# Performance work log

Measured on AMD Instinct MI355X. Metric: run time of the kernel, lower is better.

The kernel has to match this reference:

```python
import jax, jax.numpy as jnp
import numpy as np

B, S, D, H = 4096, 200, 64, 36
BN_EPS = 1e-5
DICE_EPS = 1e-3


def setup_inputs() -> dict:
    key = jax.random.key(0)
    ks = jax.random.split(key, 6)
    return {
        "history": jax.random.normal(ks[0], (B, S, D), dtype=jnp.float32),
        "candidate": jax.random.normal(ks[1], (B, D), dtype=jnp.float32),
        "W1": jax.random.normal(ks[2], (4 * D, H), dtype=jnp.float32) * 0.05,
        "b1": jax.random.normal(ks[3], (H,), dtype=jnp.float32) * 0.05,
        "gamma": jnp.ones((H,), dtype=jnp.float32),
        "beta": jnp.zeros((H,), dtype=jnp.float32),
        "alpha": jax.random.normal(ks[4], (1,), dtype=jnp.float32),
        "W2": jax.random.normal(ks[5], (H, 1), dtype=jnp.float32) * 0.05,
        "b2": jnp.zeros((1,), dtype=jnp.float32),
    }


def reference(history, candidate, W1, b1, gamma, beta, alpha, W2, b2):
    b, s, d = history.shape
    cand = jnp.broadcast_to(candidate[:, None, :], (b, s, d))
    att_in = jnp.concatenate([cand, history, cand - history, cand * history], axis=-1)
    x = att_in.reshape(b * s, 4 * d)
    # Linear
    h = x @ W1 + b1
    # BatchNorm1d (training mode: batch statistics, biased variance)
    mu = h.mean(axis=0)
    var = h.var(axis=0)
    h = (h - mu) * jax.lax.rsqrt(var + BN_EPS) * gamma + beta
    # Dice: per-row normalization over features, eps=1e-3
    avg = h.mean(axis=1, keepdims=True)
    v = jnp.sum((h - avg) ** 2, axis=1, keepdims=True) / h.shape[1]
    ps = jax.nn.sigmoid((h - avg) / jnp.sqrt(v + DICE_EPS))
    h = ps * h + (1.0 - ps) * alpha * h
    # Output linear -> attention weight per (b, s)
    w = (h @ W2 + b2).reshape(b, s)
    # Weighted sum pooling over sequence
    return jnp.einsum("bs,bsd->bd", w, history)
```

## Files before the change

kernel.cpp:

```cpp
#include <hip/hip_runtime.h>
#include <hip/hip_bf16.h>
#include <math.h>

#define BB 4096
#define SS 200
#define DD 64
#define HH 36
#define NP 48
#define NROWSF (4096.0f * 200.0f)
#define NPB (2 * BB)
#define PSTRIDE 80

typedef short bf16x8 __attribute__((ext_vector_type(8)));
typedef float f32x4 __attribute__((ext_vector_type(4)));

__device__ __forceinline__ unsigned short f2bf(float f) {
    union { float f; unsigned u; } v; v.f = f;
    unsigned r = v.u + 0x7FFFu + ((v.u >> 16) & 1u);
    return (unsigned short)(r >> 16);
}
__device__ __forceinline__ unsigned f2bf2(float a, float b) {
    union { __hip_bfloat162 h; unsigned u; } v;
    v.h = __float22bfloat162_rn(float2{a, b});
    return v.u;
}

__device__ __forceinline__ void gl_lds16(const void* g, void* l) {
    __builtin_amdgcn_global_load_lds(
        (const __attribute__((address_space(1))) unsigned*)g,
        (__attribute__((address_space(3))) unsigned*)l, 16, 0, 0);
}

__global__ __launch_bounds__(256) void k_wb(const float* __restrict__ cand,
                                            const float* __restrict__ W1,
                                            const float* __restrict__ b1,
                                            unsigned short* __restrict__ WbG,
                                            float* __restrict__ baseG) {
    int b = blockIdx.x, t = threadIdx.x;
    __shared__ float shC[DD];
    if (t < DD) shC[t] = cand[b * DD + t];
    __syncthreads();
    unsigned short* wb = WbG + (size_t)b * (NP * DD);
#pragma unroll
    for (int u = 0; u < 12; ++u) {
        int e = t + u * 256;
        int n = e >> 6, k = e & 63;
        float val = 0.f;
        if (n < HH)
            val = W1[(DD + k) * HH + n] - W1[(2 * DD + k) * HH + n] +
                  shC[k] * W1[(3 * DD + k) * HH + n];
        wb[e] = f2bf(val);
    }
    if (t < NP) {
        float v = 0.f;
        if (t < HH) {
            v = b1[t];
            for (int k = 0; k < DD; ++k)
                v += shC[k] * (W1[k * HH + t] + W1[(2 * DD + k) * HH + t]);
        }
        baseG[b * NP + t] = v;
    }
}

template <bool WB>
__device__ __forceinline__ void prologue(int b, int half, int t,
                                         const float* __restrict__ hist,
                                         const float* __restrict__ cand,
                                         const float* __restrict__ W1,
                                         const float* __restrict__ b1,
                                         const unsigned short* __restrict__ WbG,
                                         const float* __restrict__ baseG,
                                         float* shHf, unsigned short* shWbT,
                                         float* shC, float* shBase,
                                         float (*shBaseP)[NP]) {
    int w = t >> 6, l = t & 63;
    const float* hsrc = hist + ((size_t)b * SS + (half ? 112 : 0)) * DD;
    if (WB) {
        const char* hb = (const char*)hsrc;
        char* lb = (char*)shHf;
#pragma unroll
        for (int u = 0; u < 7; ++u) {
            int j = w * 7 + u;
            if (!half || j < 22)
                gl_lds16(hb + j * 1024 + l * 16, lb + j * 1024 + l * 16);
        }
        const char* wbsrc = (const char*)(WbG + (size_t)b * (NP * DD));
        char* wbl = (char*)shWbT;
        gl_lds16(wbsrc + w * 1024 + l * 16, wbl + w * 1024 + l * 16);
        if (w < 2)
            gl_lds16(wbsrc + (4 + w) * 1024 + l * 16, wbl + (4 + w) * 1024 + l * 16);
        if (t < NP) shBase[t] = baseG[b * NP + t];
        if (half && t < 128)
            *(float4*)&shHf[88 * DD + t * 4] = float4{0.f, 0.f, 0.f, 0.f};
        __syncthreads();
    } else {
        if (t < DD) shC[t] = cand[b * DD + t];
        const float4* src = (const float4*)hsrc;
        float4 v[7];
        if (!half) {
#pragma unroll
            for (int u = 0; u < 7; ++u) v[u] = src[t + u * 256];
        } else {
#pragma unroll
            for (int u = 0; u < 5; ++u) v[u] = src[t + u * 256];
            if (t < 128) v[5] = src[t + 1280];
            if (t < 128) *(float4*)&shHf[88 * DD + t * 4] = float4{0.f, 0.f, 0.f, 0.f};
        }
        __syncthreads();
#pragma unroll
        for (int u = 0; u < 7; ++u) {
            int i = t + u * 256;
            bool act = half ? (u < 5 || (u == 5 && t < 128)) : true;
            if (u < 6 || !half) {
                if (act) *(float4*)&shHf[i * 4] = v[u];
            }
        }
        for (int e = t; e < NP * DD; e += 256) {
            int n = e >> 6, k = e & 63;
            float val = 0.f;
            if (n < HH)
                val = W1[(DD + k) * HH + n] - W1[(2 * DD + k) * HH + n] +
                      shC[k] * W1[(3 * DD + k) * HH + n];
            shWbT[n * DD + k] = f2bf(val);
        }
        if (t < 4 * NP) {
            int g = t / NP, j = t - g * NP;
            float p = 0.f;
            if (j < HH) {
#pragma unroll 4
                for (int k = 16 * g; k < 16 * g + 16; ++k)
                    p += shC[k] * (W1[k * HH + j] + W1[(2 * DD + k) * HH + j]);
            }
            shBaseP[g][j] = p;
        }
        __syncthreads();
        if (t < NP) {
            float val = (t < HH) ? b1[t] : 0.f;
            shBase[t] = val + shBaseP[0][t] + shBaseP[1][t] + shBaseP[2][t] +
                        shBaseP[3][t];
        }
        __syncthreads();
    }
}

__device__ __forceinline__ void load_bfrags(const unsigned short* shWbT, int lane,
                                            bf16x8 (&bfr)[3][2]) {
    int col = lane & 15, q = lane >> 4;
#pragma unroll
    for (int nt = 0; nt < 3; ++nt)
#pragma unroll
        for (int kt = 0; kt < 2; ++kt)
            bfr[nt][kt] = *(const bf16x8*)&shWbT[(nt * 16 + col) * DD + kt * 32 + q * 8];
}

__device__ __forceinline__ bf16x8 load_afrag(const float* shHf, int m, int kt, int q) {
    const float* rp = shHf + m * DD + kt * 32 + q * 8;
    f32x4 x0 = *(const f32x4*)rp;
    f32x4 x1 = *(const f32x4*)(rp + 4);
    union { bf16x8 b8; unsigned u[4]; } a;
    a.u[0] = f2bf2(x0[0], x0[1]);
    a.u[1] = f2bf2(x0[2], x0[3]);
    a.u[2] = f2bf2(x1[0], x1[1]);
    a.u[3] = f2bf2(x1[2], x1[3]);
    return a.b8;
}

__device__ __forceinline__ void gemm_tile(const float* shHf,
                                          const bf16x8 (&bfr)[3][2], int mt, int lane,
                                          f32x4 (&d)[3]) {
    int m = mt * 16 + (lane & 15), q = lane >> 4;
    d[0] = f32x4{0.f, 0.f, 0.f, 0.f};
    d[1] = f32x4{0.f, 0.f, 0.f, 0.f};
    d[2] = f32x4{0.f, 0.f, 0.f, 0.f};
#pragma unroll
    for (int kt = 0; kt < 2; ++kt) {
        bf16x8 a = load_afrag(shHf, m, kt, q);
#pragma unroll
        for (int nt = 0; nt < 3; ++nt)
            d[nt] = __builtin_amdgcn_mfma_f32_16x16x32_bf16(a, bfr[nt][kt], d[nt], 0, 0, 0);
    }
}

template <bool WB, bool RED>
__global__ __launch_bounds__(256, 4) void k_pass1(const float* __restrict__ hist,
                                                  const float* __restrict__ cand,
                                                  const float* __restrict__ W1,
                                                  const float* __restrict__ b1,
                                                  const unsigned short* __restrict__ WbG,
                                                  const float* __restrict__ baseG,
                                                  float* __restrict__ pstat,
                                                  float* __restrict__ gsum,
                                                  float* __restrict__ gsum2) {
    __shared__ __align__(16) float shHf[112 * DD];
    __shared__ __align__(16) unsigned short shWbT[NP * DD];
    __shared__ float shC[WB ? 1 : DD], shBase[NP];
    __shared__ float shBaseP[WB ? 1 : 4][NP];
    __shared__ float shP1[4][NP], shP2[4][NP];
    int bx = blockIdx.x, b = bx >> 1, half = bx & 1;
    int t = threadIdx.x, wave = t >> 6, lane = t & 63;
    int col = lane & 15, q = lane >> 4;

    prologue<WB>(b, half, t, hist, cand, W1, b1, WbG, baseG, shHf, shWbT, shC,
                 shBase, shBaseP);

    bf16x8 bfr[3][2];
    load_bfrags(shWbT, lane, bfr);
    float basev[3];
#pragma unroll
    for (int nt = 0; nt < 3; ++nt) basev[nt] = shBase[nt * 16 + col];

    const int NTl = half ? 6 : 7;
    float cs1[3] = {0.f, 0.f, 0.f}, cs2[3] = {0.f, 0.f, 0.f};
    for (int mt = wave; mt < NTl; mt += 4) {
        f32x4 d[3];
        gemm_tile(shHf, bfr, mt, lane, d);
        if (half && mt == 5) {
            int grow0 = 192 + q * 4;
#pragma unroll
            for (int nt = 0; nt < 3; ++nt)
#pragma unroll
                for (int r = 0; r < 4; ++r)
                    if (grow0 + r < SS) {
                        float vv = d[nt][r] + basev[nt];
                        cs1[nt] += vv;
                        cs2[nt] += vv * vv;
                    }
        } else {
#pragma unroll
            for (int nt = 0; nt < 3; ++nt)
#pragma unroll
                for (int r = 0; r < 4; ++r) {
                    float vv = d[nt][r] + basev[nt];
                    cs1[nt] += vv;
                    cs2[nt] += vv * vv;
                }
        }
    }
#pragma unroll
    for (int nt = 0; nt < 3; ++nt) {
        cs1[nt] += __shfl_xor(cs1[nt], 16);
        cs1[nt] += __shfl_xor(cs1[nt], 32);
        cs2[nt] += __shfl_xor(cs2[nt], 16);
        cs2[nt] += __shfl_xor(cs2[nt], 32);
    }
    if (lane < 16) {
#pragma unroll
        for (int nt = 0; nt < 3; ++nt) {
            shP1[wave][nt * 16 + lane] = cs1[nt];
            shP2[wave][nt * 16 + lane] = cs2[nt];
        }
    }
    __syncthreads();
    if (RED) {
        if (t < HH)
            pstat[(size_t)bx * PSTRIDE + t] =
                shP1[0][t] + shP1[1][t] + shP1[2][t] + shP1[3][t];
        else if (t < 2 * HH) {
            int f = t - HH;
            pstat[(size_t)bx * PSTRIDE + t] =
                shP2[0][f] + shP2[1][f] + shP2[2][f] + shP2[3][f];
        }
    } else {
        if (t < HH) {
            atomicAdd(gsum + t, shP1[0][t] + shP1[1][t] + shP1[2][t] + shP1[3][t]);
            atomicAdd(gsum2 + t, shP2[0][t] + shP2[1][t] + shP2[2][t] + shP2[3][t]);
        }
    }
}

__global__ __launch_bounds__(256) void k_stats_red(const float* __restrict__ pstat,
                                                   const float* __restrict__ gamma,
                                                   const float* __restrict__ beta,
                                                   float* __restrict__ A,
                                                   float* __restrict__ Bc) {
    int f = blockIdx.x, t = threadIdx.x;
    if (f >= HH) {
        if (t == 0) { A[f] = 0.f; Bc[f] = 0.f; }
        return;
    }
    float s1 = 0.f, s2 = 0.f;
    for (int r = t; r < NPB; r += 256) {
        s1 += pstat[(size_t)r * PSTRIDE + f];
        s2 += pstat[(size_t)r * PSTRIDE + HH + f];
    }
#pragma unroll
    for (int off = 1; off < 64; off <<= 1) {
        s1 += __shfl_xor(s1, off);
        s2 += __shfl_xor(s2, off);
    }
    __shared__ float a1[4], a2[4];
    if ((t & 63) == 0) { a1[t >> 6] = s1; a2[t >> 6] = s2; }
    __syncthreads();
    if (t == 0) {
        s1 = a1[0] + a1[1] + a1[2] + a1[3];
        s2 = a2[0] + a2[1] + a2[2] + a2[3];
        float mu = s1 * (1.0f / NROWSF);
        float var = s2 * (1.0f / NROWSF) - mu * mu;
        float a = rsqrtf(var + 1e-5f) * gamma[f];
        A[f] = a;
        Bc[f] = beta[f] - mu * a;
    }
}

__global__ void k_stats(const float* __restrict__ gsum, const float* __restrict__ gsum2,
                        const float* __restrict__ gamma, const float* __restrict__ beta,
                        float* __restrict__ A, float* __restrict__ Bc) {
    int t = threadIdx.x;
    if (t < NP) {
        if (t < HH) {
            float mu = gsum[t] * (1.0f / NROWSF);
            float var = gsum2[t] * (1.0f / NROWSF) - mu * mu;
            float a = rsqrtf(var + 1e-5f) * gamma[t];
            A[t] = a;
            Bc[t] = beta[t] - mu * a;
        } else {
            A[t] = 0.f;
            Bc[t] = 0.f;
        }
    }
}

template <bool WB>
__global__ __launch_bounds__(256, 4) void k_pass2(const float* __restrict__ hist,
                                                  const float* __restrict__ cand,
                                                  const float* __restrict__ W1,
                                                  const float* __restrict__ b1,
                                                  const unsigned short* __restrict__ WbG,
                                                  const float* __restrict__ baseG,
                                                  const float* __restrict__ Acoef,
                                                  const float* __restrict__ Bcoef,
                                                  const float* __restrict__ alpha,
                                                  const float* __restrict__ W2,
                                                  const float* __restrict__ b2,
                                                  float* __restrict__ out) {
    __shared__ __align__(16) float shHf[112 * DD];
    __shared__ __align__(16) unsigned short shWbT[NP * DD];
    __shared__ float shC[WB ? 1 : DD], shBase[NP];
    __shared__ float shBaseP[WB ? 1 : 4][NP];
    __shared__ float shW[112];
    __shared__ float shPool[4][DD];
    int bx = blockIdx.x, b = bx >> 1, half = bx & 1;
    int t = threadIdx.x, wave = t >> 6, lane = t & 63;
    int col = lane & 15, q = lane >> 4;

    prologue<WB>(b, half, t, hist, cand, W1, b1, WbG, baseG, shHf, shWbT, shC,
                 shBase, shBaseP);

    bf16x8 bfr[3][2];
    load_bfrags(shWbT, lane, bfr);
    float baseAB[3], Ar[3], W2r[3];
#pragma unroll
    for (int nt = 0; nt < 3; ++nt) {
        int c = nt * 16 + col;
        Ar[nt] = Acoef[c];
        baseAB[nt] = fmaf(shBase[c], Ar[nt], Bcoef[c]);
        W2r[nt] = (c < HH) ? W2[c] : 0.f;
    }
    float alv = alpha[0], one_m_alv = 1.0f - alv, b2v = b2[0];

    const int NTl = half ? 6 : 7;
    for (int mt = wave; mt < NTl; mt += 4) {
        f32x4 d[3];
        gemm_tile(shHf, bfr, mt, lane, d);
        float hp[3][4];
#pragma unroll
        for (int nt = 0; nt < 3; ++nt)
#pragma unroll
            for (int r = 0; r < 4; ++r)
                hp[nt][r] = fmaf(d[nt][r], Ar[nt], baseAB[nt]);
        float s1[4], s2[4], wsum[4];
#pragma unroll
        for (int r = 0; r < 4; ++r) {
            s1[r] = hp[0][r] + hp[1][r] + hp[2][r];
            s2[r] = hp[0][r] * hp[0][r] + hp[1][r] * hp[1][r] + hp[2][r] * hp[2][r];
            s1[r] += __shfl_xor(s1[r], 1);
            s1[r] += __shfl_xor(s1[r], 2);
            s1[r] += __shfl_xor(s1[r], 4);
            s1[r] += __shfl_xor(s1[r], 8);
            s2[r] += __shfl_xor(s2[r], 1);
            s2[r] += __shfl_xor(s2[r], 2);
            s2[r] += __shfl_xor(s2[r], 4);
            s2[r] += __shfl_xor(s2[r], 8);
        }
#pragma unroll
        for (int r = 0; r < 4; ++r) {
            float avg = s1[r] * (1.0f / (float)HH);
            float var = s2[r] * (1.0f / (float)HH) - avg * avg;
            float inv = rsqrtf(var + 1e-3f);
            float wv = 0.f;
#pragma unroll
            for (int nt = 0; nt < 3; ++nt) {
                float z = (hp[nt][r] - avg) * inv;
                float ps = 1.0f / (1.0f + __expf(-z));
                float f = fmaf(ps, one_m_alv, alv);
                wv = fmaf(hp[nt][r] * f, W2r[nt], wv);
            }
            wsum[r] = wv;
            wsum[r] += __shfl_xor(wsum[r], 1);
            wsum[r] += __shfl_xor(wsum[r], 2);
            wsum[r] += __shfl_xor(wsum[r], 4);
            wsum[r] += __shfl_xor(wsum[r], 8);
        }
        if (col == 0) {
            float4 o = {wsum[0] + b2v, wsum[1] + b2v, wsum[2] + b2v, wsum[3] + b2v};
            *(float4*)&shW[mt * 16 + q * 4] = o;
        }
    }
    __syncthreads();
    {
        const int nR = half ? 88 : 112;
        float p = 0.f;
        for (int s = wave; s < nR; s += 4)
            p = fmaf(shW[s], shHf[s * DD + lane], p);
        shPool[wave][lane] = p;
    }
    __syncthreads();
    if (t < DD)
        atomicAdd(out + b * DD + t,
                  shPool[0][t] + shPool[1][t] + shPool[2][t] + shPool[3][t]);
}

extern "C" void kernel_launch(void* const* d_in, const int* in_sizes, int n_in,
                              void* d_out, int out_size, void* d_ws, size_t ws_size,
                              hipStream_t stream) {
    const float* hist = (const float*)d_in[0];
    const float* cand = (const float*)d_in[1];
    const float* W1 = (const float*)d_in[2];
    const float* b1 = (const float*)d_in[3];
    const float* gamma = (const float*)d_in[4];
    const float* beta = (const float*)d_in[5];
    const float* alpha = (const float*)d_in[6];
    const float* W2 = (const float*)d_in[7];
    const float* b2 = (const float*)d_in[8];
    float* out = (float*)d_out;
    float* ws = (float*)d_ws;

    const size_t pstatF = (size_t)NPB * PSTRIDE;
    const size_t baseF = (size_t)BB * NP;
    const size_t wbBytes = (size_t)BB * NP * DD * 2;
    const size_t fullNeed = (pstatF + 2 * NP + baseF) * 4 + wbBytes;
    const size_t midNeed = (pstatF + 2 * NP) * 4;

    hipMemsetAsync(out, 0, (size_t)out_size * sizeof(float), stream);
    if (ws_size >= fullNeed) {
        float* pstat = ws;
        float* A = pstat + pstatF;
        float* Bc = A + NP;
        float* baseG = Bc + NP;
        unsigned short* WbG = (unsigned short*)(baseG + baseF);
        k_wb<<<BB, 256, 0, stream>>>(cand, W1, b1, WbG, baseG);
        k_pass1<true, true><<<NPB, 256, 0, stream>>>(hist, cand, W1, b1, WbG, baseG,
                                                     pstat, nullptr, nullptr);
        k_stats_red<<<NP, 256, 0, stream>>>(pstat, gamma, beta, A, Bc);
        k_pass2<true><<<NPB, 256, 0, stream>>>(hist, cand, W1, b1, WbG, baseG, A, Bc,
                                               alpha, W2, b2, out);
    } else if (ws_size >= midNeed) {
        float* pstat = ws;
        float* A = pstat + pstatF;
        float* Bc = A + NP;
        k_pass1<false, true><<<NPB, 256, 0, stream>>>(hist, cand, W1, b1, nullptr,
                                                      nullptr, pstat, nullptr, nullptr);
        k_stats_red<<<NP, 256, 0, stream>>>(pstat, gamma, beta, A, Bc);
        k_pass2<false><<<NPB, 256, 0, stream>>>(hist, cand, W1, b1, nullptr, nullptr,
                                                A, Bc, alpha, W2, b2, out);
    } else {
        float* gsum = ws;
        float* gsum2 = ws + NP;
        float* A = ws + 2 * NP;
        float* Bc = ws + 3 * NP;
        hipMemsetAsync(gsum, 0, 2 * NP * sizeof(float), stream);
        k_pass1<false, false><<<NPB, 256, 0, stream>>>(hist, cand, W1, b1, nullptr,
                                                       nullptr, nullptr, gsum, gsum2);
        k_stats<<<1, 64, 0, stream>>>(gsum, gsum2, gamma, beta, A, Bc);
        k_pass2<false><<<NPB, 256, 0, stream>>>(hist, cand, W1, b1, nullptr, nullptr,
                                                A, Bc, alpha, W2, b2, out);
    }
}
```

Measured before the change: 432.9 us.

## Process each batch row in one 512-thread block instead of two half-blocks

Merges the two half-sequence blocks per batch row into a single 512-thread block that stages all 200 history rows in LDS. This removes the per-row WbG/base reload duplicated across halves, the output memset, and the atomicAdd for the pooled output, which becomes a direct store. Per-block partial statistics are halved in count. In exchange LDS per block grows to about 53KB, which may cut resident blocks per CU, and there are half as many blocks to spread the load.

```diff
diff --git a/kernel.cpp b/kernel.cpp
--- a/kernel.cpp
+++ b/kernel.cpp
@@ -7,8 +7,8 @@
 #define DD 64
 #define HH 36
 #define NP 48
+#define NTI 13
 #define NROWSF (4096.0f * 200.0f)
-#define NPB (2 * BB)
 #define PSTRIDE 80
 
 typedef short bf16x8 __attribute__((ext_vector_type(8)));
@@ -63,59 +63,44 @@
 }
 
 template <bool WB>
-__device__ __forceinline__ void prologue(int b, int half, int t,
-                                         const float* __restrict__ hist,
-                                         const float* __restrict__ cand,
-                                         const float* __restrict__ W1,
-                                         const float* __restrict__ b1,
-                                         const unsigned short* __restrict__ WbG,
-                                         const float* __restrict__ baseG,
-                                         float* shHf, unsigned short* shWbT,
-                                         float* shC, float* shBase,
-                                         float (*shBaseP)[NP]) {
-    int w = t >> 6, l = t & 63;
-    const float* hsrc = hist + ((size_t)b * SS + (half ? 112 : 0)) * DD;
+__device__ __forceinline__ void prologue512(int b, int t,
+                                            const float* __restrict__ hist,
+                                            const float* __restrict__ cand,
+                                            const float* __restrict__ W1,
+                                            const float* __restrict__ b1,
+                                            const unsigned short* __restrict__ WbG,
+                                            const float* __restrict__ baseG,
+                                            float* shHf, unsigned short* shWbT,
+                                            float* shC, float* shBase,
+                                            float (*shBaseP)[NP]) {
+    const float* hsrc = hist + (size_t)b * SS * DD;
     if (WB) {
         const char* hb = (const char*)hsrc;
         char* lb = (char*)shHf;
 #pragma unroll
-        for (int u = 0; u < 7; ++u) {
-            int j = w * 7 + u;
-            if (!half || j < 22)
-                gl_lds16(hb + j * 1024 + l * 16, lb + j * 1024 + l * 16);
-        }
+        for (int j = 0; j < 6; ++j)
+            gl_lds16(hb + (j * 512 + t) * 16, lb + (j * 512 + t) * 16);
+        if (t < 128) gl_lds16(hb + (3072 + t) * 16, lb + (3072 + t) * 16);
         const char* wbsrc = (const char*)(WbG + (size_t)b * (NP * DD));
-        char* wbl = (char*)shWbT;
-        gl_lds16(wbsrc + w * 1024 + l * 16, wbl + w * 1024 + l * 16);
-        if (w < 2)
-            gl_lds16(wbsrc + (4 + w) * 1024 + l * 16, wbl + (4 + w) * 1024 + l * 16);
+        if (t < 384) gl_lds16(wbsrc + t * 16, (char*)shWbT + t * 16);
         if (t < NP) shBase[t] = baseG[b * NP + t];
-        if (half && t < 128)
-            *(float4*)&shHf[88 * DD + t * 4] = float4{0.f, 0.f, 0.f, 0.f};
+        if (t < 128)
+            *(float4*)&shHf[SS * DD + t * 4] = float4{0.f, 0.f, 0.f, 0.f};
         __syncthreads();
     } else {
         if (t < DD) shC[t] = cand[b * DD + t];
         const float4* src = (const float4*)hsrc;
         float4 v[7];
-        if (!half) {
-#pragma unroll
-            for (int u = 0; u < 7; ++u) v[u] = src[t + u * 256];
-        } else {
-#pragma unroll
-            for (int u = 0; u < 5; ++u) v[u] = src[t + u * 256];
-            if (t < 128) v[5] = src[t + 1280];
-            if (t < 128) *(float4*)&shHf[88 * DD + t * 4] = float4{0.f, 0.f, 0.f, 0.f};
-        }
+#pragma unroll
+        for (int u = 0; u < 6; ++u) v[u] = src[t + u * 512];
+        if (t < 128) v[6] = src[t + 3072];
+        if (t < 128)
+            *(float4*)&shHf[SS * DD + t * 4] = float4{0.f, 0.f, 0.f, 0.f};
         __syncthreads();
 #pragma unroll
-        for (int u = 0; u < 7; ++u) {
-            int i = t + u * 256;
-            bool act = half ? (u < 5 || (u == 5 && t < 128)) : true;
-            if (u < 6 || !half) {
-                if (act) *(float4*)&shHf[i * 4] = v[u];
-            }
-        }
-        for (int e = t; e < NP * DD; e += 256) {
+        for (int u = 0; u < 6; ++u) *(float4*)&shHf[(t + u * 512) * 4] = v[u];
+        if (t < 128) *(float4*)&shHf[(t + 3072) * 4] = v[6];
+        for (int e = t; e < NP * DD; e += 512) {
             int n = e >> 6, k = e & 63;
             float val = 0.f;
             if (n < HH)
@@ -182,7 +167,7 @@
 }
 
 template <bool WB, bool RED>
-__global__ __launch_bounds__(256, 4) void k_pass1(const float* __restrict__ hist,
+__global__ __launch_bounds__(512, 4) void k_pass1(const float* __restrict__ hist,
                                                   const float* __restrict__ cand,
                                                   const float* __restrict__ W1,
                                                   const float* __restrict__ b1,
@@ -191,17 +176,17 @@
                                                   float* __restrict__ pstat,
                                                   float* __restrict__ gsum,
                                                   float* __restrict__ gsum2) {
-    __shared__ __align__(16) float shHf[112 * DD];
+    __shared__ __align__(16) float shHf[(SS + 8) * DD];
     __shared__ __align__(16) unsigned short shWbT[NP * DD];
     __shared__ float shC[WB ? 1 : DD], shBase[NP];
     __shared__ float shBaseP[WB ? 1 : 4][NP];
-    __shared__ float shP1[4][NP], shP2[4][NP];
-    int bx = blockIdx.x, b = bx >> 1, half = bx & 1;
+    __shared__ float shP1[8][NP], shP2[8][NP];
+    int b = blockIdx.x;
     int t = threadIdx.x, wave = t >> 6, lane = t & 63;
     int col = lane & 15, q = lane >> 4;
 
-    prologue<WB>(b, half, t, hist, cand, W1, b1, WbG, baseG, shHf, shWbT, shC,
-                 shBase, shBaseP);
+    prologue512<WB>(b, t, hist, cand, W1, b1, WbG, baseG, shHf, shWbT, shC,
+                    shBase, shBaseP);
 
     bf16x8 bfr[3][2];
     load_bfrags(shWbT, lane, bfr);
@@ -209,12 +194,11 @@
 #pragma unroll
     for (int nt = 0; nt < 3; ++nt) basev[nt] = shBase[nt * 16 + col];
 
-    const int NTl = half ? 6 : 7;
     float cs1[3] = {0.f, 0.f, 0.f}, cs2[3] = {0.f, 0.f, 0.f};
-    for (int mt = wave; mt < NTl; mt += 4) {
+    for (int mt = wave; mt < NTI; mt += 8) {
         f32x4 d[3];
         gemm_tile(shHf, bfr, mt, lane, d);
-        if (half && mt == 5) {
+        if (mt == 12) {
             int grow0 = 192 + q * 4;
 #pragma unroll
             for (int nt = 0; nt < 3; ++nt)
@@ -252,18 +236,25 @@
     }
     __syncthreads();
     if (RED) {
-        if (t < HH)
-            pstat[(size_t)bx * PSTRIDE + t] =
-                shP1[0][t] + shP1[1][t] + shP1[2][t] + shP1[3][t];
-        else if (t < 2 * HH) {
+        if (t < HH) {
+            float s = 0.f;
+#pragma unroll
+            for (int w = 0; w < 8; ++w) s += shP1[w][t];
+            pstat[(size_t)b * PSTRIDE + t] = s;
+        } else if (t < 2 * HH) {
             int f = t - HH;
-            pstat[(size_t)bx * PSTRIDE + t] =
-                shP2[0][f] + shP2[1][f] + shP2[2][f] + shP2[3][f];
+            float s = 0.f;
+#pragma unroll
+            for (int w = 0; w < 8; ++w) s += shP2[w][f];
+            pstat[(size_t)b * PSTRIDE + t] = s;
         }
     } else {
         if (t < HH) {
-            atomicAdd(gsum + t, shP1[0][t] + shP1[1][t] + shP1[2][t] + shP1[3][t]);
-            atomicAdd(gsum2 + t, shP2[0][t] + shP2[1][t] + shP2[2][t] + shP2[3][t]);
+            float s1 = 0.f, s2 = 0.f;
+#pragma unroll
+            for (int w = 0; w < 8; ++w) { s1 += shP1[w][t]; s2 += shP2[w][t]; }
+            atomicAdd(gsum + t, s1);
+            atomicAdd(gsum2 + t, s2);
         }
     }
 }
@@ -279,7 +270,7 @@
         return;
     }
     float s1 = 0.f, s2 = 0.f;
-    for (int r = t; r < NPB; r += 256) {
+    for (int r = t; r < BB; r += 256) {
         s1 += pstat[(size_t)r * PSTRIDE + f];
         s2 += pstat[(size_t)r * PSTRIDE + HH + f];
     }
@@ -321,7 +312,7 @@
 }
 
 template <bool WB>
-__global__ __launch_bounds__(256, 4) void k_pass2(const float* __restrict__ hist,
+__global__ __launch_bounds__(512, 4) void k_pass2(const float* __restrict__ hist,
                                                   const float* __restrict__ cand,
                                                   const float* __restrict__ W1,
                                                   const float* __restrict__ b1,
@@ -333,18 +324,18 @@
                                                   const float* __restrict__ W2,
                                                   const float* __restrict__ b2,
                                                   float* __restrict__ out) {
-    __shared__ __align__(16) float shHf[112 * DD];
+    __shared__ __align__(16) float shHf[(SS + 8) * DD];
     __shared__ __align__(16) unsigned short shWbT[NP * DD];
     __shared__ float shC[WB ? 1 : DD], shBase[NP];
     __shared__ float shBaseP[WB ? 1 : 4][NP];
-    __shared__ float shW[112];
-    __shared__ float shPool[4][DD];
-    int bx = blockIdx.x, b = bx >> 1, half = bx & 1;
+    __shared__ float shW[(SS + 8)];
+    __shared__ float shPool[8][DD];
+    int b = blockIdx.x;
     int t = threadIdx.x, wave = t >> 6, lane = t & 63;
     int col = lane & 15, q = lane >> 4;
 
-    prologue<WB>(b, half, t, hist, cand, W1, b1, WbG, baseG, shHf, shWbT, shC,
-                 shBase, shBaseP);
+    prologue512<WB>(b, t, hist, cand, W1, b1, WbG, baseG, shHf, shWbT, shC,
+                    shBase, shBaseP);
 
     bf16x8 bfr[3][2];
     load_bfrags(shWbT, lane, bfr);
@@ -358,8 +349,7 @@
     }
     float alv = alpha[0], one_m_alv = 1.0f - alv, b2v = b2[0];
 
-    const int NTl = half ? 6 : 7;
-    for (int mt = wave; mt < NTl; mt += 4) {
+    for (int mt = wave; mt < NTI; mt += 8) {
         f32x4 d[3];
         gemm_tile(shHf, bfr, mt, lane, d);
         float hp[3][4];
@@ -408,16 +398,18 @@
     }
     __syncthreads();
     {
-        const int nR = half ? 88 : 112;
         float p = 0.f;
-        for (int s = wave; s < nR; s += 4)
+        for (int s = wave; s < SS; s += 8)
             p = fmaf(shW[s], shHf[s * DD + lane], p);
         shPool[wave][lane] = p;
     }
     __syncthreads();
-    if (t < DD)
-        atomicAdd(out + b * DD + t,
-                  shPool[0][t] + shPool[1][t] + shPool[2][t] + shPool[3][t]);
+    if (t < DD) {
+        float s = 0.f;
+#pragma unroll
+        for (int w = 0; w < 8; ++w) s += shPool[w][t];
+        out[b * DD + t] = s;
+    }
 }
 
 extern "C" void kernel_launch(void* const* d_in, const int* in_sizes, int n_in,
@@ -435,13 +427,12 @@
     float* out = (float*)d_out;
     float* ws = (float*)d_ws;
 
-    const size_t pstatF = (size_t)NPB * PSTRIDE;
+    const size_t pstatF = (size_t)BB * PSTRIDE;
     const size_t baseF = (size_t)BB * NP;
     const size_t wbBytes = (size_t)BB * NP * DD * 2;
     const size_t fullNeed = (pstatF + 2 * NP + baseF) * 4 + wbBytes;
     const size_t midNeed = (pstatF + 2 * NP) * 4;
 
-    hipMemsetAsync(out, 0, (size_t)out_size * sizeof(float), stream);
     if (ws_size >= fullNeed) {
         float* pstat = ws;
         float* A = pstat + pstatF;
@@ -449,30 +440,30 @@
         float* baseG = Bc + NP;
         unsigned short* WbG = (unsigned short*)(baseG + baseF);
         k_wb<<<BB, 256, 0, stream>>>(cand, W1, b1, WbG, baseG);
-        k_pass1<true, true><<<NPB, 256, 0, stream>>>(hist, cand, W1, b1, WbG, baseG,
-                                                     pstat, nullptr, nullptr);
+        k_pass1<true, true><<<BB, 512, 0, stream>>>(hist, cand, W1, b1, WbG, baseG,
+                                                    pstat, nullptr, nullptr);
         k_stats_red<<<NP, 256, 0, stream>>>(pstat, gamma, beta, A, Bc);
-        k_pass2<true><<<NPB, 256, 0, stream>>>(hist, cand, W1, b1, WbG, baseG, A, Bc,
-                                               alpha, W2, b2, out);
+        k_pass2<true><<<BB, 512, 0, stream>>>(hist, cand, W1, b1, WbG, baseG, A, Bc,
+                                              alpha, W2, b2, out);
     } else if (ws_size >= midNeed) {
         float* pstat = ws;
         float* A = pstat + pstatF;
         float* Bc = A + NP;
-        k_pass1<false, true><<<NPB, 256, 0, stream>>>(hist, cand, W1, b1, nullptr,
-                                                      nullptr, pstat, nullptr, nullptr);
+        k_pass1<false, true><<<BB, 512, 0, stream>>>(hist, cand, W1, b1, nullptr,
+                                                     nullptr, pstat, nullptr, nullptr);
         k_stats_red<<<NP, 256, 0, stream>>>(pstat, gamma, beta, A, Bc);
-        k_pass2<false><<<NPB, 256, 0, stream>>>(hist, cand, W1, b1, nullptr, nullptr,
-                                                A, Bc, alpha, W2, b2, out);
+        k_pass2<false><<<BB, 512, 0, stream>>>(hist, cand, W1, b1, nullptr, nullptr,
+                                               A, Bc, alpha, W2, b2, out);
     } else {
         float* gsum = ws;
         float* gsum2 = ws + NP;
         float* A = ws + 2 * NP;
         float* Bc = ws + 3 * NP;
         hipMemsetAsync(gsum, 0, 2 * NP * sizeof(float), stream);
-        k_pass1<false, false><<<NPB, 256, 0, stream>>>(hist, cand, W1, b1, nullptr,
-                                                       nullptr, nullptr, gsum, gsum2);
+        k_pass1<false, false><<<BB, 512, 0, stream>>>(hist, cand, W1, b1, nullptr,
+                                                      nullptr, nullptr, gsum, gsum2);
         k_stats<<<1, 64, 0, stream>>>(gsum, gsum2, gamma, beta, A, Bc);
-        k_pass2<false><<<NPB, 256, 0, stream>>>(hist, cand, W1, b1, nullptr, nullptr,
-                                                A, Bc, alpha, W2, b2, out);
-    }
-}
+        k_pass2<false><<<BB, 512, 0, stream>>>(hist, cand, W1, b1, nullptr, nullptr,
+                                               A, Bc, alpha, W2, b2, out);
+    }
+}
```

Measured after the change: 418.5 us. -3.3%, faster.
